# Performance work log

Hardware: AMD Instinct MI355X
Metric: run time of the kernel (lower is better)

The kernel has to match this reference:

```python
import jax, jax.numpy as jnp
import numpy as np

N = 100000   # nodes
E = 3200000  # edges
CY = 128     # channels_y (signal length per node)
HID = 10     # hidden_channels
H = 2        # heads
C = 10       # out channels per head
BN_EPS = 1e-5


def _glorot(k, shape):
    lim = float(np.sqrt(6.0 / (shape[0] + shape[1])))
    return jax.random.uniform(k, shape, jnp.float32, -lim, lim)


def setup_inputs() -> dict:
    key = jax.random.key(0)
    ks = jax.random.split(key, 16)
    p = {}
    p["signal"] = jax.random.normal(ks[0], (N, CY), jnp.float32)
    p["edge_index"] = jax.random.randint(ks[1], (2, E), 0, N)
    p["edge_weight"] = jax.random.uniform(ks[2], (E,), jnp.float32)
    p["mask"] = jax.random.bernoulli(ks[3], 0.3, (N,))
    # mlp_in: Linear(CY,512) -> BatchNorm -> ReLU -> Linear(512,HID) (PyG MLP, plain_last)
    p["W1"] = _glorot(ks[4], (CY, 512)); p["b1"] = jnp.zeros((512,), jnp.float32)
    p["gamma"] = jnp.ones((512,), jnp.float32); p["beta"] = jnp.zeros((512,), jnp.float32)
    p["W2"] = _glorot(ks[5], (512, HID)); p["b2"] = jnp.zeros((HID,), jnp.float32)
    # GATv2Conv(HID, HID, heads=2, edge_dim=1, concat=True)
    p["Wl"] = _glorot(ks[6], (HID, H * C)); p["bl"] = jnp.zeros((H * C,), jnp.float32)
    p["Wr"] = _glorot(ks[7], (HID, H * C)); p["br"] = jnp.zeros((H * C,), jnp.float32)
    p["We"] = _glorot(ks[8], (1, H * C))              # lin_edge, no bias
    p["att"] = _glorot(ks[9], (H, C))                 # attention vector per head
    p["gat_bias"] = jnp.zeros((H * C,), jnp.float32)
    # mlp_out: MLP([20,512]) single layer, plain_last -> just Linear (dropout off in eval)
    p["W3"] = _glorot(ks[10], (H * C, 512)); p["b3"] = jnp.zeros((512,), jnp.float32)
    # out_linear: Linear(512, CY)
    p["W4"] = _glorot(ks[11], (512, CY)); p["b4"] = jnp.zeros((CY,), jnp.float32)
    return p


def _forward(signal, edge_index, edge_weight, mask,
             W1, b1, gamma, beta, W2, b2,
             Wl, bl, Wr, br, We, att, gat_bias,
             W3, b3, W4, b4):
    # node masking: (signal.T * ~mask).T
    x = signal * (~mask)[:, None].astype(signal.dtype)
    # mlp_in (eval mode: BN with running mean=0, var=1)
    x = x @ W1 + b1
    x = x * (gamma / jnp.sqrt(jnp.asarray(1.0 + BN_EPS, x.dtype))) + beta
    x = jax.nn.relu(x)
    x = x @ W2 + b2                                   # [N, HID]
    # GATv2Conv
    src, dst = edge_index[0], edge_index[1]
    xl = (x @ Wl + bl).reshape(N, H, C)               # source transform
    xr = (x @ Wr + br).reshape(N, H, C)               # target transform
    ea = (edge_weight[:, None] @ We).reshape(E, H, C)  # edge feature transform
    e = jax.nn.leaky_relu(xl[src] + xr[dst] + ea, 0.2)  # [E,H,C]
    alpha = jnp.einsum('ehc,hc->eh', e, att)          # [E,H]
    # segment softmax over incoming edges of each dst node
    m = jax.ops.segment_max(alpha, dst, num_segments=N)
    ex = jnp.exp(alpha - m[dst])
    den = jax.ops.segment_sum(ex, dst, num_segments=N)
    a = ex / (den[dst] + 1e-16)                       # [E,H]
    out = jax.ops.segment_sum(xl[src] * a[:, :, None], dst, num_segments=N)
    out = out.reshape(N, H * C) + gat_bias            # concat heads + bias
    # mlp_out (single plain-last layer) + out_linear
    out = out @ W3 + b3
    out = out @ W4 + b4
    return out


def reference(signal, edge_index, edge_weight, mask,
              W1, b1, gamma, beta, W2, b2,
              Wl, bl, Wr, br, We, att, gat_bias,
              W3, b3, W4, b4):
    return _forward(signal, edge_index, edge_weight, mask,
                    W1, b1, gamma, beta, W2, b2,
                    Wl, bl, Wr, br, We, att, gat_bias,
                    W3, b3, W4, b4)
```

## Files before the change

### kernel.cpp

```cpp
#include <hip/hip_runtime.h>
#include <hip/hip_bf16.h>

constexpr int NN = 100000;
constexpr int NE = 3200000;
constexpr int CYC = 128;
constexpr int NB = 1563;
constexpr int EBLK = 256;
constexpr int ECHUNK = NE / EBLK;
constexpr int MSCAN = NB * EBLK;
constexpr int CAP = 2432;
constexpr int NBLK_A = (NN + 63) / 64;

#define OFF_W1T    0u
#define OFF_W2T    131072u
#define OFF_B1E    147456u
#define OFF_SMALL  149504u
#define OFF_W34    151808u
#define OFF_B34    162048u
#define OFF_FLAGS  162560u
#define OFF_XLB    163840u
#define OFF_XR     6563840u
#define OFF_GH     14563840u
#define OFF_BB     16164352u
#define OFF_BS     16170752u
#define OFF_BIN    16171776u

#define SF_WLR 0
#define SF_BLR 400
#define SF_ATT 440
#define SF_WE  460
#define SF_GB  480
#define SF_B2  500

typedef __attribute__((ext_vector_type(8))) short bf16x8;
typedef __attribute__((ext_vector_type(4))) float f32x4;

__device__ __forceinline__ float bfu(unsigned short x) {
  return __uint_as_float(((unsigned)x) << 16);
}
__device__ __forceinline__ short f2bf(float f) {
  __hip_bfloat16 h = __float2bfloat16(f);
  return *reinterpret_cast<short*>(&h);
}
__device__ __forceinline__ float LD(const void* p, long i, int f32f) {
  return f32f ? ((const float*)p)[i] : bfu(((const unsigned short*)p)[i]);
}

__global__ __launch_bounds__(256) void kPrep(
    const void* __restrict__ W1, const void* __restrict__ b1,
    const void* __restrict__ gamma, const void* __restrict__ beta,
    const void* __restrict__ W2, const void* __restrict__ b2,
    const void* __restrict__ Wl, const void* __restrict__ bl,
    const void* __restrict__ Wr, const void* __restrict__ br,
    const void* __restrict__ We, const void* __restrict__ att,
    const void* __restrict__ gbias, const void* __restrict__ W3,
    const void* __restrict__ b3, const void* __restrict__ W4,
    const void* __restrict__ b4, const void* __restrict__ mask,
    int* __restrict__ flags,
    short* __restrict__ W1T, float* __restrict__ b1eff, short* __restrict__ W2T,
    float* __restrict__ smallf, float* __restrict__ W34, float* __restrict__ b34)
{
  __shared__ int sfl[2];
  int t = threadIdx.x;
  if (t < 64) {
    const unsigned short* W1u = (const unsigned short*)W1;
    const unsigned* masku = (const unsigned*)mask;
    int big = 0;
#pragma unroll
    for (int k = 0; k < 8; k++) {
      unsigned e = (W1u[t * 8 + k] >> 7) & 0xFF;
      if (e >= 170) big++;
    }
    int byt = 0;
#pragma unroll
    for (int k = 0; k < 4; k++) if (masku[t * 4 + k] & ~1u) byt = 1;
#pragma unroll
    for (int o = 1; o < 64; o <<= 1) {
      big += __shfl_xor(big, o);
      byt |= __shfl_xor(byt, o);
    }
    if (t == 0) {
      sfl[0] = (big >= 4) ? 1 : 0;
      sfl[1] = byt;
      if (blockIdx.x == 0) { flags[0] = sfl[0]; flags[1] = byt; }
    }
  }
  __syncthreads();
  const int f32f = sfl[0];

  int tid = blockIdx.x * 256 + t;
  const float rs = 0.999995000037f;
  if (tid < 65536) {
    int j = tid >> 7, k = tid & 127;
    float s = LD(gamma, j, f32f) * rs;
    W1T[j * 128 + k] = f2bf(LD(W1, k * 512 + j, f32f) * s);
    if (k == 0) b1eff[j] = LD(b1, j, f32f) * s + LD(beta, j, f32f);
  } else if (tid < 73728) {
    int i = tid - 65536;
    int c = i >> 9, k = i & 511;
    W2T[c * 512 + k] = (c < 10) ? f2bf(LD(W2, k * 10 + c, f32f)) : (short)0;
  } else if (tid < 76288) {
    int i = tid - 73728;
    int j = i >> 7, tt = i & 127;
    float acc = 0.f;
    for (int k = 0; k < 512; k++) acc += LD(W3, j * 512 + k, f32f) * LD(W4, k * 128 + tt, f32f);
    W34[j * 128 + tt] = acc;
  } else if (tid < 76416) {
    int tt = tid - 76288;
    float acc = LD(b4, tt, f32f);
    for (int k = 0; k < 512; k++) acc += LD(b3, k, f32f) * LD(W4, k * 128 + tt, f32f);
    b34[tt] = acc;
  } else if (tid < 76932) {
    int i = tid - 76416;
    if (i < 400) {
      int c = i / 40, o = i % 40;
      smallf[SF_WLR + i] = (o < 20) ? LD(Wl, c * 20 + o, f32f) : LD(Wr, c * 20 + (o - 20), f32f);
    } else if (i < 440) {
      int o = i - 400;
      smallf[SF_BLR + o] = (o < 20) ? LD(bl, o, f32f) : LD(br, o - 20, f32f);
    } else if (i < 460) {
      smallf[SF_ATT + (i - 440)] = LD(att, i - 440, f32f);
    } else if (i < 480) {
      smallf[SF_WE + (i - 460)] = LD(We, i - 460, f32f);
    } else if (i < 500) {
      smallf[SF_GB + (i - 480)] = LD(gbias, i - 480, f32f);
    } else {
      int c = i - 500;
      smallf[SF_B2 + c] = (c < 10) ? LD(b2, c, f32f) : 0.f;
    }
  }
}

__global__ __launch_bounds__(256, 2) void kA(
    const void* __restrict__ sig, const void* __restrict__ mask,
    const short* __restrict__ W1T, const float* __restrict__ b1eff,
    const short* __restrict__ W2T, const float* __restrict__ smallf,
    const int* __restrict__ flags,
    unsigned short* __restrict__ xlb, float* __restrict__ xr)
{
  __shared__ __align__(16) char sR1[17408];
  __shared__ short sH[4][32 * 136];
  __shared__ float sb1[512];
  __shared__ float sxh[64][12];
  __shared__ float sWlr[400];
  __shared__ float sblr[40];
  __shared__ float sb2[16];

  short (*sA)[136]        = (short (*)[136])sR1;
  float (*sxhp)[64][17]   = (float (*)[64][17])sR1;
  float (*sxlr)[40]       = (float (*)[40])sR1;

  const int f32f = flags[0];
  const int mk8  = flags[1];
  int t = threadIdx.x;
  int w = t >> 6, l = t & 63;
  int lrow = l & 15, quad = l >> 4;
  int row0 = blockIdx.x * 64;

  for (int i = t; i < 512; i += 256) sb1[i] = b1eff[i];
  for (int i = t; i < 400; i += 256) sWlr[i] = smallf[SF_WLR + i];
  if (t < 40) sblr[t] = smallf[SF_BLR + t];
  if (t < 16) sb2[t] = smallf[SF_B2 + t];

  bf16x8 zz = {0, 0, 0, 0, 0, 0, 0, 0};
#pragma unroll
  for (int k = 0; k < 4; k++) {
    int idx = t + k * 256;
    int row = idx >> 4, seg = idx & 15;
    int gr = row0 + row;
    int grc = gr < NN ? gr : NN - 1;
    bool mbit = mk8 ? (((const unsigned char*)mask)[grc] != 0)
                    : (((const int*)mask)[grc] != 0);
    bf16x8 v;
    if (mbit) {
      v = zz;
    } else if (f32f) {
      const float4* Sf = (const float4*)((const float*)sig + (size_t)grc * CYC) + seg * 2;
      float4 x0 = Sf[0], x1 = Sf[1];
      v[0] = f2bf(x0.x); v[1] = f2bf(x0.y); v[2] = f2bf(x0.z); v[3] = f2bf(x0.w);
      v[4] = f2bf(x1.x); v[5] = f2bf(x1.y); v[6] = f2bf(x1.z); v[7] = f2bf(x1.w);
    } else {
      v = ((const bf16x8*)((const unsigned short*)sig + (size_t)grc * CYC))[seg];
    }
    *(bf16x8*)&sA[row][seg * 8] = v;
  }
  __syncthreads();

  float bcol[8];
#pragma unroll
  for (int ct = 0; ct < 8; ct++) bcol[ct] = sb1[w * 128 + ct * 16 + lrow];

  f32x4 acc[4][8];
#pragma unroll
  for (int rf = 0; rf < 4; rf++)
#pragma unroll
    for (int ct = 0; ct < 8; ct++) acc[rf][ct] = (f32x4){0.f, 0.f, 0.f, 0.f};

  const bf16x8* Bp = (const bf16x8*)W1T;
  int bvbase = w * 2048 + lrow * 16 + quad;
#pragma unroll
  for (int kt = 0; kt < 4; kt++) {
    bf16x8 a0 = *(const bf16x8*)&sA[lrow][kt * 32 + quad * 8];
    bf16x8 a1 = *(const bf16x8*)&sA[16 + lrow][kt * 32 + quad * 8];
    bf16x8 a2f = *(const bf16x8*)&sA[32 + lrow][kt * 32 + quad * 8];
    bf16x8 a3 = *(const bf16x8*)&sA[48 + lrow][kt * 32 + quad * 8];
#pragma unroll
    for (int ct = 0; ct < 8; ct++) {
      bf16x8 bv = Bp[bvbase + ct * 256 + kt * 4];
      acc[0][ct] = __builtin_amdgcn_mfma_f32_16x16x32_bf16(a0, bv, acc[0][ct], 0, 0, 0);
      acc[1][ct] = __builtin_amdgcn_mfma_f32_16x16x32_bf16(a1, bv, acc[1][ct], 0, 0, 0);
      acc[2][ct] = __builtin_amdgcn_mfma_f32_16x16x32_bf16(a2f, bv, acc[2][ct], 0, 0, 0);
      acc[3][ct] = __builtin_amdgcn_mfma_f32_16x16x32_bf16(a3, bv, acc[3][ct], 0, 0, 0);
    }
  }
  __syncthreads();

  const bf16x8* B2p = (const bf16x8*)W2T;
  bf16x8 b2v[4];
#pragma unroll
  for (int kt2 = 0; kt2 < 4; kt2++) b2v[kt2] = B2p[lrow * 64 + w * 16 + kt2 * 4 + quad];

  short* hb = &sH[w][0];
#pragma unroll
  for (int hf = 0; hf < 2; hf++) {
#pragma unroll
    for (int rr = 0; rr < 2; rr++) {
      int rf = hf * 2 + rr;
#pragma unroll
      for (int ct = 0; ct < 8; ct++) {
        float bb = bcol[ct];
#pragma unroll
        for (int r = 0; r < 4; r++) {
          float vv = fmaxf(acc[rf][ct][r] + bb, 0.f);
          hb[(rr * 16 + quad * 4 + r) * 136 + ct * 16 + lrow] = f2bf(vv);
        }
      }
    }
    asm volatile("s_waitcnt lgkmcnt(0)" ::: "memory");

    f32x4 a2[2];
    a2[0] = (f32x4){0.f, 0.f, 0.f, 0.f};
    a2[1] = (f32x4){0.f, 0.f, 0.f, 0.f};
#pragma unroll
    for (int kt2 = 0; kt2 < 4; kt2++) {
      bf16x8 x0 = *(const bf16x8*)&hb[lrow * 136 + kt2 * 32 + quad * 8];
      bf16x8 x1 = *(const bf16x8*)&hb[(16 + lrow) * 136 + kt2 * 32 + quad * 8];
      a2[0] = __builtin_amdgcn_mfma_f32_16x16x32_bf16(x0, b2v[kt2], a2[0], 0, 0, 0);
      a2[1] = __builtin_amdgcn_mfma_f32_16x16x32_bf16(x1, b2v[kt2], a2[1], 0, 0, 0);
    }
#pragma unroll
    for (int f = 0; f < 2; f++)
#pragma unroll
      for (int r = 0; r < 4; r++)
        sxhp[w][hf * 32 + f * 16 + quad * 4 + r][lrow] = a2[f][r];
  }
  __syncthreads();

  for (int i = t; i < 640; i += 256) {
    int row = i / 10, c = i - row * 10;
    sxh[row][c] = sxhp[0][row][c] + sxhp[1][row][c] + sxhp[2][row][c] + sxhp[3][row][c] + sb2[c];
  }
  __syncthreads();

  for (int i = t; i < 2560; i += 256) {
    int row = i / 40, o = i - row * 40;
    float v = sblr[o];
#pragma unroll
    for (int c = 0; c < 10; c++) v += sxh[row][c] * sWlr[c * 40 + o];
    sxlr[row][o] = v;
  }
  __syncthreads();

  int nrows = NN - row0; if (nrows > 64) nrows = 64;
  unsigned* xlb32 = (unsigned*)xlb;
#pragma unroll
  for (int k = 0; k < 4; k++) {
    int i = t + k * 256;
    int row = i >> 4, p = i & 15;
    if (row < nrows) {
      int s0 = 2 * p, s1 = 2 * p + 1;
      float lo = (s0 < 10) ? sxlr[row][s0] : (s0 >= 16 && s0 < 26) ? sxlr[row][s0 - 6] : 0.f;
      float hi = (s1 < 10) ? sxlr[row][s1] : (s1 >= 16 && s1 < 26) ? sxlr[row][s1 - 6] : 0.f;
      unsigned u = (unsigned)(unsigned short)f2bf(lo) |
                   ((unsigned)(unsigned short)f2bf(hi) << 16);
      xlb32[(size_t)(row0 + row) * 16 + p] = u;
    }
  }
#pragma unroll
  for (int k = 0; k < 5; k++) {
    int i = t + k * 256;
    int row = i / 20, c = i - row * 20;
    if (row < nrows) xr[(size_t)(row0 + row) * 20 + c] = sxlr[row][20 + c];
  }
}

__global__ __launch_bounds__(256) void kB1(const int* __restrict__ ei,
                                           int* __restrict__ gh) {
  __shared__ int h[NB];
  int t = threadIdx.x, blk = blockIdx.x;
  for (int i = t; i < NB; i += 256) h[i] = 0;
  __syncthreads();
  const int* dst = ei + NE;
  int base = blk * ECHUNK, bend = base + ECHUNK;
  for (int i = base + t; i < bend; i += 256)
    atomicAdd(&h[dst[i] >> 6], 1);
  __syncthreads();
  for (int i = t; i < NB; i += 256) gh[i * EBLK + blk] = h[i];
}

__global__ __launch_bounds__(256) void kS1(const int* __restrict__ gh,
                                           int* __restrict__ ghx,
                                           int* __restrict__ bsum) {
  __shared__ int sS[256];
  int t = threadIdx.x;
  int base = blockIdx.x * 2048 + t * 8;
  int d[8], tsum = 0;
#pragma unroll
  for (int k = 0; k < 8; k++) {
    d[k] = (base + k < MSCAN) ? gh[base + k] : 0;
    tsum += d[k];
  }
  sS[t] = tsum;
  __syncthreads();
  for (int o = 1; o < 256; o <<= 1) {
    int v = (t >= o) ? sS[t - o] : 0;
    __syncthreads();
    sS[t] += v;
    __syncthreads();
  }
  int run = sS[t] - tsum;
#pragma unroll
  for (int k = 0; k < 8; k++) {
    if (base + k < MSCAN) ghx[base + k] = run;
    run += d[k];
  }
  if (t == 255) bsum[blockIdx.x] = sS[255];
}

__global__ __launch_bounds__(256) void kS2(int* __restrict__ bsum, int nb) {
  __shared__ int sS[256];
  int t = threadIdx.x;
  int v = (t < nb) ? bsum[t] : 0;
  sS[t] = v;
  __syncthreads();
  for (int o = 1; o < 256; o <<= 1) {
    int u = (t >= o) ? sS[t - o] : 0;
    __syncthreads();
    sS[t] += u;
    __syncthreads();
  }
  if (t < nb) bsum[t] = sS[t] - v;
}

__global__ __launch_bounds__(256) void kS3(int* __restrict__ gh,
                                           const int* __restrict__ bsum,
                                           int* __restrict__ bb) {
  int i = blockIdx.x * 256 + threadIdx.x;
  int v = gh[i] + bsum[i >> 11];
  gh[i] = v;
  if ((i & 255) == 0) bb[i >> 8] = v;
  if (i == 0) bb[NB] = NE;
}

__global__ __launch_bounds__(256) void kB3(const int* __restrict__ ei,
                                           const void* __restrict__ ew,
                                           const int* __restrict__ flags,
                                           const int* __restrict__ gh,
                                           int2* __restrict__ binned) {
  __shared__ int cur[NB];
  const int f32f = flags[0];
  int t = threadIdx.x, blk = blockIdx.x;
  for (int i = t; i < NB; i += 256) cur[i] = gh[i * EBLK + blk];
  __syncthreads();
  int base = blk * ECHUNK, bend = base + ECHUNK;
  for (int i = base + t; i < bend; i += 256) {
    int s = ei[i], d = ei[NE + i];
    float w = LD(ew, i, f32f);
    int b = d >> 6;
    int pos = atomicAdd(&cur[b], 1);
    binned[pos] = make_int2(s | ((d & 63) << 17), __float_as_int(w));
  }
}

__global__ __launch_bounds__(256) void kSrtAgg(
    const int* __restrict__ bb, const int2* __restrict__ binned,
    const unsigned short* __restrict__ xlb, const float* __restrict__ xr,
    const float* __restrict__ smallf, const float* __restrict__ W34,
    const float* __restrict__ b34, const int* __restrict__ flags,
    void* __restrict__ out)
{
  __shared__ int2  sES[CAP];
  __shared__ float sXr[64 * 20];
  __shared__ float sW[2560];
  __shared__ int   sCnt[64];
  __shared__ int   sPre[64];
  __shared__ int   sStart[64];
  __shared__ int   sCur[64];
  __shared__ float sb[128];
  __shared__ float sAtt[20], sWe[20], sGb[20];

  const int f32f = flags[0];
  int t = threadIdx.x, b = blockIdx.x;
  int node0 = b * 64;

  for (int i = t; i < 2560; i += 256) sW[i] = W34[i];
  for (int i = t; i < 1280; i += 256) {
    int gi = node0 * 20 + i;
    sXr[i] = (gi < NN * 20) ? xr[gi] : 0.f;
  }
  if (t < 128) sb[t] = b34[t];
  if (t < 64) sCnt[t] = 0;
  if (t < 20) { sAtt[t] = smallf[SF_ATT + t]; sWe[t] = smallf[SF_WE + t]; sGb[t] = smallf[SF_GB + t]; }
  __syncthreads();

  int base = bb[b], end = bb[b + 1];
  int ne = end - base;

  for (int i = t; i < ne; i += 256)
    atomicAdd(&sCnt[(unsigned)binned[base + i].x >> 17], 1);
  __syncthreads();

  if (t < 64) sPre[t] = sCnt[t];
  __syncthreads();
  for (int o = 1; o < 64; o <<= 1) {
    int v = 0;
    if (t < 64 && t >= o) v = sPre[t - o];
    __syncthreads();
    if (t < 64) sPre[t] += v;
    __syncthreads();
  }
  if (t < 64) {
    int ex = sPre[t] - sCnt[t];
    sStart[t] = ex;
    sCur[t] = ex;
  }
  __syncthreads();

  for (int i = t; i < ne; i += 256) {
    int2 e = binned[base + i];
    int dl = (unsigned)e.x >> 17;
    int pos = atomicAdd(&sCur[dl], 1);
    if (pos < CAP) sES[pos] = make_int2(e.x & 0x1FFFF, e.y);
  }
  __syncthreads();

  int n = t >> 2, head = (t >> 1) & 1, part = t & 1;
  float xrw[10], attw[10], wew[10];
#pragma unroll
  for (int c = 0; c < 10; c++) {
    xrw[c]  = sXr[n * 20 + head * 10 + c];
    attw[c] = sAtt[head * 10 + c];
    wew[c]  = sWe[head * 10 + c];
  }
  float acc[10];
#pragma unroll
  for (int c = 0; c < 10; c++) acc[c] = 0.f;
  float den = 0.f;
  int s0 = sStart[n];
  int s1 = s0 + sCnt[n];
  if (s1 > CAP) s1 = CAP;
  for (int i = s0 + part; i < s1; i += 2) {
    int2 e = sES[i];
    const unsigned short* p = xlb + (size_t)e.x * 32 + head * 16;
    uint4 q = *(const uint4*)p;
    unsigned q4 = *(const unsigned*)(p + 8);
    float vl[10];
    unsigned qq[5] = {q.x, q.y, q.z, q.w, q4};
#pragma unroll
    for (int k = 0; k < 5; k++) {
      vl[2 * k]     = __uint_as_float(qq[k] << 16);
      vl[2 * k + 1] = __uint_as_float(qq[k] & 0xffff0000u);
    }
    float ww = __int_as_float(e.y);
    float a = 0.f;
#pragma unroll
    for (int c = 0; c < 10; c++) {
      float v = vl[c] + xrw[c] + ww * wew[c];
      v = fmaxf(v, 0.2f * v);
      a += v * attw[c];
    }
    float pp = __expf(a);
    den += pp;
#pragma unroll
    for (int c = 0; c < 10; c++) acc[c] += pp * vl[c];
  }
  den += __shfl_xor(den, 1);
#pragma unroll
  for (int c = 0; c < 10; c++) acc[c] += __shfl_xor(acc[c], 1);

  __syncthreads();
  if (part == 0) {
    float inv = 1.f / (den + 1e-16f);
#pragma unroll
    for (int c = 0; c < 10; c++)
      sXr[n * 20 + head * 10 + c] = acc[c] * inv + sGb[head * 10 + c];
  }
  __syncthreads();

  int col = t & 127, half = t >> 7;
  for (int n2 = half; n2 < 64; n2 += 2) {
    int gn = node0 + n2;
    if (gn >= NN) break;
    float v = sb[col];
    const float* g = &sXr[n2 * 20];
#pragma unroll
    for (int c = 0; c < 20; c++) v += g[c] * sW[c * 128 + col];
    if (f32f) ((float*)out)[(size_t)gn * 128 + col] = v;
    else ((unsigned short*)out)[(size_t)gn * 128 + col] = (unsigned short)f2bf(v);
  }
}

extern "C" void kernel_launch(void* const* d_in, const int* in_sizes, int n_in,
                              void* d_out, int out_size, void* d_ws, size_t ws_size,
                              hipStream_t stream) {
  (void)in_sizes; (void)n_in; (void)out_size; (void)ws_size;
  const void* sig  = d_in[0];
  const int*  ei   = (const int*)d_in[1];
  const void* ew   = d_in[2];
  const void* mask = d_in[3];
  const void* W1   = d_in[4];
  const void* b1   = d_in[5];
  const void* gam  = d_in[6];
  const void* bet  = d_in[7];
  const void* W2   = d_in[8];
  const void* b2   = d_in[9];
  const void* Wl   = d_in[10];
  const void* bl   = d_in[11];
  const void* Wr   = d_in[12];
  const void* br   = d_in[13];
  const void* We   = d_in[14];
  const void* att  = d_in[15];
  const void* gb   = d_in[16];
  const void* W3   = d_in[17];
  const void* b3   = d_in[18];
  const void* W4   = d_in[19];
  const void* b4   = d_in[20];

  char* ws = (char*)d_ws;
  short* W1T    = (short*)(ws + OFF_W1T);
  short* W2T    = (short*)(ws + OFF_W2T);
  float* b1eff  = (float*)(ws + OFF_B1E);
  float* smallf = (float*)(ws + OFF_SMALL);
  float* W34    = (float*)(ws + OFF_W34);
  float* b34    = (float*)(ws + OFF_B34);
  int*   flags  = (int*)(ws + OFF_FLAGS);
  unsigned short* xlb = (unsigned short*)(ws + OFF_XLB);
  float* xr     = (float*)(ws + OFF_XR);
  int*   gh     = (int*)(ws + OFF_GH);
  int*   bb     = (int*)(ws + OFF_BB);
  int*   bsum   = (int*)(ws + OFF_BS);
  int2*  bincsr = (int2*)(ws + OFF_BIN);

  kPrep<<<301, 256, 0, stream>>>(W1, b1, gam, bet, W2, b2, Wl, bl, Wr, br, We, att,
                                 gb, W3, b3, W4, b4, mask, flags,
                                 W1T, b1eff, W2T, smallf, W34, b34);
  kA<<<NBLK_A, 256, 0, stream>>>(sig, mask, W1T, b1eff, W2T, smallf, flags, xlb, xr);
  kB1<<<EBLK, 256, 0, stream>>>(ei, gh);
  kS1<<<(MSCAN + 2047) / 2048, 256, 0, stream>>>(gh, gh, bsum);
  kS2<<<1, 256, 0, stream>>>(bsum, (MSCAN + 2047) / 2048);
  kS3<<<NB, 256, 0, stream>>>(gh, bsum, bb);
  kB3<<<EBLK, 256, 0, stream>>>(ei, ew, flags, gh, bincsr);
  kSrtAgg<<<NB, 256, 0, stream>>>(bb, bincsr, xlb, xr, smallf, W34, b34, flags, d_out);
}
```

Measured before the change: 448.0 us.

## Split sort and aggregation kernels, prefetch gathers, parallelize W34 fold, shrink kA LDS

The fused sort+aggregate kernel becomes two kernels. kSort writes a node-sorted CSR back to global memory along with per-node start offsets, and kAgg reads that CSR and software-prefetches the next edge's source features. The W3·W4 and b3·W4 folds in kPrep are now split over 16 lanes with a shuffle reduction, using more blocks. kA handles one 16-row fragment at a time, halving sH, and raises its occupancy hint to 3. The trade-off is an extra global round trip for the sorted edges and one more kernel launch, in exchange for smaller LDS use and more overlap of the gather latency.

```diff
diff --git a/kernel.cpp b/kernel.cpp
--- a/kernel.cpp
+++ b/kernel.cpp
@@ -20,10 +20,11 @@
 #define OFF_FLAGS  162560u
 #define OFF_XLB    163840u
 #define OFF_XR     6563840u
-#define OFF_GH     14563840u
-#define OFF_BB     16164352u
-#define OFF_BS     16170752u
-#define OFF_BIN    16171776u
+#define OFF_NS     14563840u
+#define OFF_GH     14965248u
+#define OFF_BB     16565760u
+#define OFF_BS     16572160u
+#define OFF_BIN    16573184u
 
 #define SF_WLR 0
 #define SF_BLR 400
@@ -99,19 +100,27 @@
     int i = tid - 65536;
     int c = i >> 9, k = i & 511;
     W2T[c * 512 + k] = (c < 10) ? f2bf(LD(W2, k * 10 + c, f32f)) : (short)0;
-  } else if (tid < 76288) {
+  } else if (tid < 114688) {
     int i = tid - 73728;
-    int j = i >> 7, tt = i & 127;
+    int o = i >> 4, k0 = i & 15;
+    int j = o >> 7, tt = o & 127;
     float acc = 0.f;
-    for (int k = 0; k < 512; k++) acc += LD(W3, j * 512 + k, f32f) * LD(W4, k * 128 + tt, f32f);
-    W34[j * 128 + tt] = acc;
-  } else if (tid < 76416) {
-    int tt = tid - 76288;
-    float acc = LD(b4, tt, f32f);
-    for (int k = 0; k < 512; k++) acc += LD(b3, k, f32f) * LD(W4, k * 128 + tt, f32f);
-    b34[tt] = acc;
-  } else if (tid < 76932) {
-    int i = tid - 76416;
+    for (int k = k0; k < 512; k += 16)
+      acc += LD(W3, j * 512 + k, f32f) * LD(W4, k * 128 + tt, f32f);
+#pragma unroll
+    for (int o2 = 1; o2 < 16; o2 <<= 1) acc += __shfl_xor(acc, o2);
+    if (k0 == 0) W34[o] = acc;
+  } else if (tid < 116736) {
+    int i = tid - 114688;
+    int tt = i >> 4, k0 = i & 15;
+    float acc = 0.f;
+    for (int k = k0; k < 512; k += 16)
+      acc += LD(b3, k, f32f) * LD(W4, k * 128 + tt, f32f);
+#pragma unroll
+    for (int o2 = 1; o2 < 16; o2 <<= 1) acc += __shfl_xor(acc, o2);
+    if (k0 == 0) b34[tt] = acc + LD(b4, tt, f32f);
+  } else if (tid < 117252) {
+    int i = tid - 116736;
     if (i < 400) {
       int c = i / 40, o = i % 40;
       smallf[SF_WLR + i] = (o < 20) ? LD(Wl, c * 20 + o, f32f) : LD(Wr, c * 20 + (o - 20), f32f);
@@ -131,7 +140,7 @@
   }
 }
 
-__global__ __launch_bounds__(256, 2) void kA(
+__global__ __launch_bounds__(256, 3) void kA(
     const void* __restrict__ sig, const void* __restrict__ mask,
     const short* __restrict__ W1T, const float* __restrict__ b1eff,
     const short* __restrict__ W2T, const float* __restrict__ smallf,
@@ -139,7 +148,7 @@
     unsigned short* __restrict__ xlb, float* __restrict__ xr)
 {
   __shared__ __align__(16) char sR1[17408];
-  __shared__ short sH[4][32 * 136];
+  __shared__ short sH[4][16 * 136];
   __shared__ float sb1[512];
   __shared__ float sxh[64][12];
   __shared__ float sWlr[400];
@@ -222,37 +231,27 @@
 
   short* hb = &sH[w][0];
 #pragma unroll
-  for (int hf = 0; hf < 2; hf++) {
-#pragma unroll
-    for (int rr = 0; rr < 2; rr++) {
-      int rf = hf * 2 + rr;
-#pragma unroll
-      for (int ct = 0; ct < 8; ct++) {
-        float bb = bcol[ct];
-#pragma unroll
-        for (int r = 0; r < 4; r++) {
-          float vv = fmaxf(acc[rf][ct][r] + bb, 0.f);
-          hb[(rr * 16 + quad * 4 + r) * 136 + ct * 16 + lrow] = f2bf(vv);
-        }
+  for (int qf = 0; qf < 4; qf++) {
+#pragma unroll
+    for (int ct = 0; ct < 8; ct++) {
+      float bb = bcol[ct];
+#pragma unroll
+      for (int r = 0; r < 4; r++) {
+        float vv = fmaxf(acc[qf][ct][r] + bb, 0.f);
+        hb[(quad * 4 + r) * 136 + ct * 16 + lrow] = f2bf(vv);
       }
     }
     asm volatile("s_waitcnt lgkmcnt(0)" ::: "memory");
 
-    f32x4 a2[2];
-    a2[0] = (f32x4){0.f, 0.f, 0.f, 0.f};
-    a2[1] = (f32x4){0.f, 0.f, 0.f, 0.f};
+    f32x4 a2 = (f32x4){0.f, 0.f, 0.f, 0.f};
 #pragma unroll
     for (int kt2 = 0; kt2 < 4; kt2++) {
       bf16x8 x0 = *(const bf16x8*)&hb[lrow * 136 + kt2 * 32 + quad * 8];
-      bf16x8 x1 = *(const bf16x8*)&hb[(16 + lrow) * 136 + kt2 * 32 + quad * 8];
-      a2[0] = __builtin_amdgcn_mfma_f32_16x16x32_bf16(x0, b2v[kt2], a2[0], 0, 0, 0);
-      a2[1] = __builtin_amdgcn_mfma_f32_16x16x32_bf16(x1, b2v[kt2], a2[1], 0, 0, 0);
-    }
-#pragma unroll
-    for (int f = 0; f < 2; f++)
-#pragma unroll
-      for (int r = 0; r < 4; r++)
-        sxhp[w][hf * 32 + f * 16 + quad * 4 + r][lrow] = a2[f][r];
+      a2 = __builtin_amdgcn_mfma_f32_16x16x32_bf16(x0, b2v[kt2], a2, 0, 0, 0);
+    }
+#pragma unroll
+    for (int r = 0; r < 4; r++)
+      sxhp[w][qf * 16 + quad * 4 + r][lrow] = a2[r];
   }
   __syncthreads();
 
@@ -308,16 +307,16 @@
   for (int i = t; i < NB; i += 256) gh[i * EBLK + blk] = h[i];
 }
 
-__global__ __launch_bounds__(256) void kS1(const int* __restrict__ gh,
-                                           int* __restrict__ ghx,
-                                           int* __restrict__ bsum) {
+__global__ __launch_bounds__(256) void kS1(const int* __restrict__ in,
+                                           int* __restrict__ outx,
+                                           int* __restrict__ bsum, int nelem) {
   __shared__ int sS[256];
   int t = threadIdx.x;
   int base = blockIdx.x * 2048 + t * 8;
   int d[8], tsum = 0;
 #pragma unroll
   for (int k = 0; k < 8; k++) {
-    d[k] = (base + k < MSCAN) ? gh[base + k] : 0;
+    d[k] = (base + k < nelem) ? in[base + k] : 0;
     tsum += d[k];
   }
   sS[t] = tsum;
@@ -331,7 +330,7 @@
   int run = sS[t] - tsum;
 #pragma unroll
   for (int k = 0; k < 8; k++) {
-    if (base + k < MSCAN) ghx[base + k] = run;
+    if (base + k < nelem) outx[base + k] = run;
     run += d[k];
   }
   if (t == 255) bsum[blockIdx.x] = sS[255];
@@ -382,44 +381,23 @@
   }
 }
 
-__global__ __launch_bounds__(256) void kSrtAgg(
-    const int* __restrict__ bb, const int2* __restrict__ binned,
-    const unsigned short* __restrict__ xlb, const float* __restrict__ xr,
-    const float* __restrict__ smallf, const float* __restrict__ W34,
-    const float* __restrict__ b34, const int* __restrict__ flags,
-    void* __restrict__ out)
-{
-  __shared__ int2  sES[CAP];
-  __shared__ float sXr[64 * 20];
-  __shared__ float sW[2560];
-  __shared__ int   sCnt[64];
-  __shared__ int   sPre[64];
-  __shared__ int   sStart[64];
-  __shared__ int   sCur[64];
-  __shared__ float sb[128];
-  __shared__ float sAtt[20], sWe[20], sGb[20];
-
-  const int f32f = flags[0];
+__global__ __launch_bounds__(256) void kSort(const int* __restrict__ bb,
+                                             int2* __restrict__ binned,
+                                             int* __restrict__ nstart) {
+  __shared__ int2 sRaw[CAP];
+  __shared__ int sCnt[64], sPre[64], sCur[64];
   int t = threadIdx.x, b = blockIdx.x;
-  int node0 = b * 64;
-
-  for (int i = t; i < 2560; i += 256) sW[i] = W34[i];
-  for (int i = t; i < 1280; i += 256) {
-    int gi = node0 * 20 + i;
-    sXr[i] = (gi < NN * 20) ? xr[gi] : 0.f;
-  }
-  if (t < 128) sb[t] = b34[t];
-  if (t < 64) sCnt[t] = 0;
-  if (t < 20) { sAtt[t] = smallf[SF_ATT + t]; sWe[t] = smallf[SF_WE + t]; sGb[t] = smallf[SF_GB + t]; }
-  __syncthreads();
-
   int base = bb[b], end = bb[b + 1];
   int ne = end - base;
-
-  for (int i = t; i < ne; i += 256)
-    atomicAdd(&sCnt[(unsigned)binned[base + i].x >> 17], 1);
-  __syncthreads();
-
+  if (ne > CAP) ne = CAP;
+  if (t < 64) sCnt[t] = 0;
+  __syncthreads();
+  for (int i = t; i < ne; i += 256) {
+    int2 e = binned[base + i];
+    sRaw[i] = e;
+    atomicAdd(&sCnt[(unsigned)e.x >> 17], 1);
+  }
+  __syncthreads();
   if (t < 64) sPre[t] = sCnt[t];
   __syncthreads();
   for (int o = 1; o < 64; o <<= 1) {
@@ -431,17 +409,44 @@
   }
   if (t < 64) {
     int ex = sPre[t] - sCnt[t];
-    sStart[t] = ex;
     sCur[t] = ex;
-  }
-  __syncthreads();
-
+    nstart[b * 64 + t] = base + ex;
+  }
+  if (t == 63 && b == NB - 1) nstart[NB * 64] = base + sPre[63];
+  __syncthreads();
   for (int i = t; i < ne; i += 256) {
-    int2 e = binned[base + i];
+    int2 e = sRaw[i];
     int dl = (unsigned)e.x >> 17;
     int pos = atomicAdd(&sCur[dl], 1);
-    if (pos < CAP) sES[pos] = make_int2(e.x & 0x1FFFF, e.y);
-  }
+    binned[base + pos] = make_int2(e.x & 0x1FFFF, e.y);
+  }
+}
+
+__global__ __launch_bounds__(256) void kAgg(
+    const int* __restrict__ nstart, const int2* __restrict__ binned,
+    const unsigned short* __restrict__ xlb, const float* __restrict__ xr,
+    const float* __restrict__ smallf, const float* __restrict__ W34,
+    const float* __restrict__ b34, const int* __restrict__ flags,
+    void* __restrict__ out)
+{
+  __shared__ float sXr[64 * 20];
+  __shared__ float sW[2560];
+  __shared__ float sb[128];
+  __shared__ int   sStart[65];
+  __shared__ float sAtt[20], sWe[20], sGb[20];
+
+  const int f32f = flags[0];
+  int t = threadIdx.x, b = blockIdx.x;
+  int node0 = b * 64;
+
+  for (int i = t; i < 2560; i += 256) sW[i] = W34[i];
+  for (int i = t; i < 1280; i += 256) {
+    int gi = node0 * 20 + i;
+    sXr[i] = (gi < NN * 20) ? xr[gi] : 0.f;
+  }
+  if (t < 128) sb[t] = b34[t];
+  if (t < 65) sStart[t] = nstart[node0 + t];
+  if (t < 20) { sAtt[t] = smallf[SF_ATT + t]; sWe[t] = smallf[SF_WE + t]; sGb[t] = smallf[SF_GB + t]; }
   __syncthreads();
 
   int n = t >> 2, head = (t >> 1) & 1, part = t & 1;
@@ -456,14 +461,25 @@
 #pragma unroll
   for (int c = 0; c < 10; c++) acc[c] = 0.f;
   float den = 0.f;
-  int s0 = sStart[n];
-  int s1 = s0 + sCnt[n];
-  if (s1 > CAP) s1 = CAP;
-  for (int i = s0 + part; i < s1; i += 2) {
-    int2 e = sES[i];
+  int s0 = sStart[n], s1 = sStart[n + 1];
+
+  int i = s0 + part;
+  int2 e; uint4 q; unsigned q4;
+  if (i < s1) {
+    e = binned[i];
     const unsigned short* p = xlb + (size_t)e.x * 32 + head * 16;
-    uint4 q = *(const uint4*)p;
-    unsigned q4 = *(const unsigned*)(p + 8);
+    q = *(const uint4*)p;
+    q4 = *(const unsigned*)(p + 8);
+  }
+  while (i < s1) {
+    int j = i + 2;
+    int2 en; uint4 qn; unsigned qn4;
+    if (j < s1) {
+      en = binned[j];
+      const unsigned short* pn = xlb + (size_t)en.x * 32 + head * 16;
+      qn = *(const uint4*)pn;
+      qn4 = *(const unsigned*)(pn + 8);
+    }
     float vl[10];
     unsigned qq[5] = {q.x, q.y, q.z, q.w, q4};
 #pragma unroll
@@ -483,6 +499,7 @@
     den += pp;
 #pragma unroll
     for (int c = 0; c < 10; c++) acc[c] += pp * vl[c];
+    e = en; q = qn; q4 = qn4; i = j;
   }
   den += __shfl_xor(den, 1);
 #pragma unroll
@@ -546,19 +563,21 @@
   int*   flags  = (int*)(ws + OFF_FLAGS);
   unsigned short* xlb = (unsigned short*)(ws + OFF_XLB);
   float* xr     = (float*)(ws + OFF_XR);
+  int*   nstart = (int*)(ws + OFF_NS);
   int*   gh     = (int*)(ws + OFF_GH);
   int*   bb     = (int*)(ws + OFF_BB);
   int*   bsum   = (int*)(ws + OFF_BS);
   int2*  bincsr = (int2*)(ws + OFF_BIN);
 
-  kPrep<<<301, 256, 0, stream>>>(W1, b1, gam, bet, W2, b2, Wl, bl, Wr, br, We, att,
+  kPrep<<<459, 256, 0, stream>>>(W1, b1, gam, bet, W2, b2, Wl, bl, Wr, br, We, att,
                                  gb, W3, b3, W4, b4, mask, flags,
                                  W1T, b1eff, W2T, smallf, W34, b34);
   kA<<<NBLK_A, 256, 0, stream>>>(sig, mask, W1T, b1eff, W2T, smallf, flags, xlb, xr);
   kB1<<<EBLK, 256, 0, stream>>>(ei, gh);
-  kS1<<<(MSCAN + 2047) / 2048, 256, 0, stream>>>(gh, gh, bsum);
+  kS1<<<(MSCAN + 2047) / 2048, 256, 0, stream>>>(gh, gh, bsum, MSCAN);
   kS2<<<1, 256, 0, stream>>>(bsum, (MSCAN + 2047) / 2048);
   kS3<<<NB, 256, 0, stream>>>(gh, bsum, bb);
   kB3<<<EBLK, 256, 0, stream>>>(ei, ew, flags, gh, bincsr);
-  kSrtAgg<<<NB, 256, 0, stream>>>(bb, bincsr, xlb, xr, smallf, W34, b34, flags, d_out);
-}
+  kSort<<<NB, 256, 0, stream>>>(bb, bincsr, nstart);
+  kAgg<<<NB, 256, 0, stream>>>(nstart, bincsr, xlb, xr, smallf, W34, b34, flags, d_out);
+}
```

New measurement: 481.3 us. 1.07x slower.
